# Optimization experiments

Hardware: AMD Instinct MI355X
Metric: run time of the kernel (lower is better)

Reference implementation:

```python
import math
import jax, jax.numpy as jnp
import numpy as np

LOW_FREQ = 1
FACTOR = 1


def setup_inputs() -> dict:
    key = jax.random.key(0)
    x = jax.random.normal(key, (16, 4096, 256), dtype=jnp.float32)
    return {"x": x}


def reference(x):
    b, t, d = x.shape
    x_freq = jnp.fft.rfft(x, axis=1)  # (b, t//2+1, d) complex
    if t % 2 == 0:
        x_freq = x_freq[:, LOW_FREQ:-1]
        f = jnp.fft.rfftfreq(t)[LOW_FREQ:-1]
    else:
        x_freq = x_freq[:, LOW_FREQ:]
        f = jnp.fft.rfftfreq(t)[LOW_FREQ:]
    f = f.astype(jnp.float32)
    F = x_freq.shape[1]
    top_k = int(FACTOR * math.log(F))  # static (shape-derived)

    # top-k by magnitude along freq axis, independently per (b, d)
    xf_bdf = jnp.moveaxis(x_freq, 1, 2)              # (b, d, F)
    _, idx = jax.lax.top_k(jnp.abs(xf_bdf), top_k)   # (b, d, k) int32
    xf_sel = jnp.take_along_axis(xf_bdf, idx, axis=2)  # (b, d, k)
    xf_sel = jnp.moveaxis(xf_sel, 2, 1)              # (b, k, d)
    f_sel = jnp.moveaxis(f[idx], 2, 1)[:, :, None, :]  # (b, k, 1, d)

    # extrapolate: conj-pair frequencies, synthesize cosines, reduce over freq
    xf2 = jnp.concatenate([xf_sel, jnp.conj(xf_sel)], axis=1)  # (b, 2k, d)
    f2 = jnp.concatenate([f_sel, -f_sel], axis=1)              # (b, 2k, 1, d)
    tt = jnp.arange(t, dtype=jnp.float32)[None, None, :, None]  # (1,1,t,1)
    amp = (jnp.abs(xf2) * 2.0 / t)[:, :, None, :]   # (b, 2k, 1, d)
    phase = jnp.angle(xf2)[:, :, None, :]           # (b, 2k, 1, d)
    x_time = amp * jnp.cos(2.0 * math.pi * f2 * tt + phase)  # (b, 2k, t, d)
    return x_time.sum(axis=1)  # (b, t, d)
```

## Files before the change

kernel.cpp:

```cpp
#include <hip/hip_runtime.h>
#include <math.h>

#define T_LEN 4096
#define N2    2048
#define TOPK  7
#define NCH   256
#define R8 0.70710678118654752440

#define AD(a) ((a) + ((a) >> 3) + ((a) >> 8))

__global__ __launch_bounds__(256) void prep_kernel(
    const float* __restrict__ x, float* __restrict__ xt, double2* __restrict__ tw)
{
    if (blockIdx.x < 16) {
        int p = blockIdx.x * 256 + threadIdx.x;
        double th = -2.0 * 3.14159265358979323846 * (double)p / (double)T_LEN;
        tw[p] = make_double2(cos(th), sin(th));
        return;
    }
    __shared__ float tile[64][65];
    const int bid = blockIdx.x - 16;
    const int t0  = (bid & 63) * 64;
    const int c0  = ((bid >> 6) & 3) * 64;
    const int b   = bid >> 8;
    const int tx4 = (threadIdx.x & 15) * 4;
    const int ty  = threadIdx.x >> 4;

    const float* src = x + (size_t)b * T_LEN * NCH;
    for (int r = 0; r < 4; ++r) {
        int t = ty + r * 16;
        float4 v = *(const float4*)(src + (size_t)(t0 + t) * NCH + c0 + tx4);
        tile[t][tx4 + 0] = v.x; tile[t][tx4 + 1] = v.y;
        tile[t][tx4 + 2] = v.z; tile[t][tx4 + 3] = v.w;
    }
    __syncthreads();
    float* dst = xt + (size_t)b * NCH * T_LEN;
    for (int r = 0; r < 4; ++r) {
        int c = ty + r * 16;
        float4 v = make_float4(tile[tx4 + 0][c], tile[tx4 + 1][c],
                               tile[tx4 + 2][c], tile[tx4 + 3][c]);
        *(float4*)(dst + (size_t)(c0 + c) * T_LEN + t0 + tx4) = v;
    }
}

__device__ __forceinline__ void dft8_tw(double ar[8], double ai[8],
                                        int base, const double2* __restrict__ tw)
{
    double t0r=ar[0]+ar[4], t0i=ai[0]+ai[4], t4r=ar[0]-ar[4], t4i=ai[0]-ai[4];
    double t1r=ar[1]+ar[5], t1i=ai[1]+ai[5], t5r=ar[1]-ar[5], t5i=ai[1]-ai[5];
    double t2r=ar[2]+ar[6], t2i=ai[2]+ai[6], t6r=ar[2]-ar[6], t6i=ai[2]-ai[6];
    double t3r=ar[3]+ar[7], t3i=ai[3]+ai[7], t7r=ar[3]-ar[7], t7i=ai[3]-ai[7];
    double s0r=t0r+t2r, s0i=t0i+t2i, s2r=t0r-t2r, s2i=t0i-t2i;
    double s1r=t1r+t3r, s1i=t1i+t3i, s3r=t1r-t3r, s3i=t1i-t3i;
    ar[0]=s0r+s1r; ai[0]=s0i+s1i;
    ar[4]=s0r-s1r; ai[4]=s0i-s1i;
    ar[2]=s2r+s3i; ai[2]=s2i-s3r;
    ar[6]=s2r-s3i; ai[6]=s2i+s3r;
    double c1r=R8*(t5r+t5i), c1i=R8*(t5i-t5r);
    double c2r=t6i,          c2i=-t6r;
    double c3r=R8*(t7i-t7r), c3i=-R8*(t7r+t7i);
    double d0r=t4r+c2r, d0i=t4i+c2i, d1r=t4r-c2r, d1i=t4i-c2i;
    double d2r=c1r+c3r, d2i=c1i+c3i, d3r=c1r-c3r, d3i=c1i-c3i;
    ar[1]=d0r+d2r; ai[1]=d0i+d2i;
    ar[5]=d0r-d2r; ai[5]=d0i-d2i;
    ar[3]=d1r+d3i; ai[3]=d1i-d3r;
    ar[7]=d1r-d3i; ai[7]=d1i+d3r;
#pragma unroll
    for (int m = 1; m < 8; ++m) {
        double2 w = tw[(base * m) & 4095];
        double xr = ar[m], xi = ai[m];
        ar[m] = w.x * xr - w.y * xi;
        ai[m] = w.x * xi + w.y * xr;
    }
}

__device__ __forceinline__ unsigned long long packkey(double mag, int k) {
    unsigned long long b = __double_as_longlong(mag);
    return (b & ~2047ULL) | (unsigned long long)(2047 - k);
}

__global__ __launch_bounds__(256, 4) void fft_topk_kernel(
    const float* __restrict__ xt, const double2* __restrict__ tw,
    int* __restrict__ k_out, float4* __restrict__ ab4)
{
    __shared__ double2 zz[AD(N2 - 1) + 3];
    __shared__ unsigned long long kshare[256];
    __shared__ unsigned long long selkey[TOPK];

    const int tid = threadIdx.x;
    const int bc  = blockIdx.x;
    const float2* xcol2 = (const float2*)(xt + (size_t)bc * T_LEN);

    double ar[8], ai[8];
#pragma unroll
    for (int u = 0; u < 8; ++u) {
        float2 v = xcol2[tid + (u << 8)];
        ar[u] = (double)v.x; ai[u] = (double)v.y;
    }
    dft8_tw(ar, ai, 2 * tid, tw);
#pragma unroll
    for (int m = 0; m < 8; ++m)
        zz[AD((m << 8) + tid)] = make_double2(ar[m], ai[m]);
    __syncthreads();

    {
        const int g = tid >> 5, j2 = tid & 31, base = (g << 8) + j2;
#pragma unroll
        for (int u = 0; u < 8; ++u) {
            double2 v = zz[AD(base + (u << 5))];
            ar[u] = v.x; ai[u] = v.y;
        }
        dft8_tw(ar, ai, 16 * j2, tw);
#pragma unroll
        for (int m = 0; m < 8; ++m)
            zz[AD(base + (m << 5))] = make_double2(ar[m], ai[m]);
    }
    __syncthreads();

    {
        const int g3 = tid >> 2, j3 = tid & 3, base = (g3 << 5) + j3;
#pragma unroll
        for (int u = 0; u < 8; ++u) {
            double2 v = zz[AD(base + (u << 2))];
            ar[u] = v.x; ai[u] = v.y;
        }
        dft8_tw(ar, ai, 128 * j3, tw);
#pragma unroll
        for (int m = 0; m < 8; ++m)
            zz[AD(base + (m << 2))] = make_double2(ar[m], ai[m]);
    }
    __syncthreads();

#pragma unroll
    for (int q = 0; q < 2; ++q) {
        int h4 = ((q << 8) + tid) << 2;
#pragma unroll
        for (int r = 0; r < 4; ++r) {
            double2 v = zz[AD(h4 + r)];
            ar[q * 4 + r] = v.x; ai[q * 4 + r] = v.y;
        }
    }
    __syncthreads();
#pragma unroll
    for (int q = 0; q < 2; ++q) {
        double b0r = ar[q*4+0], b0i = ai[q*4+0], b1r = ar[q*4+1], b1i = ai[q*4+1];
        double b2r = ar[q*4+2], b2i = ai[q*4+2], b3r = ar[q*4+3], b3i = ai[q*4+3];
        double e0r = b0r + b2r, e0i = b0i + b2i, e1r = b0r - b2r, e1i = b0i - b2i;
        double e2r = b1r + b3r, e2i = b1i + b3i, e3r = b1r - b3r, e3i = b1i - b3i;
        int kbase = ((tid & 7) << 6) | (((tid >> 3) & 7) << 3) | (q << 2) | (tid >> 6);
        zz[AD(kbase)]        = make_double2(e0r + e2r, e0i + e2i);
        zz[AD(kbase + 1024)] = make_double2(e0r - e2r, e0i - e2i);
        zz[AD(kbase +  512)] = make_double2(e1r + e3i, e1i - e3r);
        zz[AD(kbase + 1536)] = make_double2(e1r - e3i, e1i + e3r);
    }
    __syncthreads();

    unsigned long long keys[8];
#pragma unroll
    for (int j = 0; j < 4; ++j) {
        int k  = 1 + tid + (j << 8);
        int kp = N2 - k;
        double2 yk = zz[AD(k)];
        double2 yp = zz[AD(kp)];
        double Ar = 0.5 * (yk.x + yp.x), Ai = 0.5 * (yk.y - yp.y);
        double Br = 0.5 * (yk.y + yp.y), Bi = -0.5 * (yk.x - yp.x);
        double2 t = tw[k];
        double Cr = t.x * Br - t.y * Bi;
        double Ci = t.x * Bi + t.y * Br;
        double m1 = (Ar + Cr) * (Ar + Cr) + (Ai + Ci) * (Ai + Ci);
        double m2 = (Ar - Cr) * (Ar - Cr) + (Ai - Ci) * (Ai - Ci);
        keys[2 * j]     = packkey(m1, k);
        keys[2 * j + 1] = (kp != k) ? packkey(m2, kp) : 0ULL;
    }

    unsigned long long lb = 0ULL;
#pragma unroll
    for (int s = 0; s < 8; ++s) lb = (keys[s] > lb) ? keys[s] : lb;

    for (int it = 0; it < TOPK; ++it) {
        kshare[tid] = lb;
        __syncthreads();
        if (tid < 64) {
            unsigned long long v = kshare[tid];
            unsigned long long v1 = kshare[tid + 64];  if (v1 > v) v = v1;
            unsigned long long v2 = kshare[tid + 128]; if (v2 > v) v = v2;
            unsigned long long v3 = kshare[tid + 192]; if (v3 > v) v = v3;
#pragma unroll
            for (int off = 32; off; off >>= 1) {
                unsigned long long o = __shfl_down(v, off);
                if (o > v) v = o;
            }
            if (tid == 0) selkey[it] = v;
        }
        __syncthreads();
        unsigned long long w = selkey[it];
        if (w == lb) {
#pragma unroll
            for (int s = 0; s < 8; ++s) if (keys[s] == w) keys[s] = 0ULL;
            lb = 0ULL;
#pragma unroll
            for (int s = 0; s < 8; ++s) lb = (keys[s] > lb) ? keys[s] : lb;
        }
    }

    if (tid < TOPK) {
        int k  = 2047 - (int)(selkey[tid] & 2047ULL);
        double2 yk = zz[AD(k)];
        double2 yp = zz[AD(N2 - k)];
        double Ar = 0.5 * (yk.x + yp.x), Ai = 0.5 * (yk.y - yp.y);
        double Br = 0.5 * (yk.y + yp.y), Bi = -0.5 * (yk.x - yp.x);
        double2 t = tw[k];
        double Xr = Ar + t.x * Br - t.y * Bi;
        double Xi = Ai + t.x * Bi + t.y * Br;
        k_out[tid * 4096 + bc] = k;
        ab4[tid * 4096 + bc] = make_float4(
            (float)( 4.0 * Xr / (double)T_LEN),
            (float)(-4.0 * Xi / (double)T_LEN),
            (float)t.x, (float)(-t.y));
    }
}

__global__ __launch_bounds__(256) void recon_kernel(
    const int* __restrict__ k_in, const float4* __restrict__ ab4,
    float* __restrict__ out)
{
    __shared__ float tile[16][256];

    const int tid   = threadIdx.x;
    const int chunk = blockIdx.x & 127;
    const int b     = blockIdx.x >> 7;
    const int bc    = (b << 8) + tid;
    const int n0    = chunk << 5;

    const float c0 = 6.28318530717958647692f / 4096.0f;
    float aa[TOPK], bb[TOPK], zr[TOPK], zi[TOPK], wr[TOPK], wi[TOPK];
#pragma unroll
    for (int j = 0; j < TOPK; ++j) {
        int k    = k_in[j * 4096 + bc];
        float4 v = ab4[j * 4096 + bc];
        aa[j] = v.x; bb[j] = v.y; wr[j] = v.z; wi[j] = v.w;
        int m0 = (k * n0) & (T_LEN - 1);
        float ang = (float)m0 * c0;
        zr[j] = __cosf(ang);
        zi[j] = __sinf(ang);
    }

    float* obase = out + ((size_t)b * T_LEN + n0) * NCH;
    for (int r = 0; r < 2; ++r) {
#pragma unroll
        for (int i = 0; i < 16; ++i) {
            float acc = 0.f;
#pragma unroll
            for (int j = 0; j < TOPK; ++j) {
                acc += aa[j] * zr[j] + bb[j] * zi[j];
                float nzr = zr[j] * wr[j] - zi[j] * wi[j];
                zi[j] = zr[j] * wi[j] + zi[j] * wr[j];
                zr[j] = nzr;
            }
            tile[i][tid] = acc;
        }
        __syncthreads();
#pragma unroll
        for (int s = 0; s < 4; ++s) {
            int fid = tid + (s << 8);
            int ni  = fid >> 6;
            int c4  = (fid & 63) << 2;
            float4 v = make_float4(tile[ni][c4], tile[ni][c4 + 1],
                                   tile[ni][c4 + 2], tile[ni][c4 + 3]);
            *(float4*)(obase + (size_t)((r << 4) + ni) * NCH + c4) = v;
        }
        __syncthreads();
    }
}

extern "C" void kernel_launch(void* const* d_in, const int* in_sizes, int n_in,
                              void* d_out, int out_size, void* d_ws, size_t ws_size,
                              hipStream_t stream) {
    const float* x   = (const float*)d_in[0];
    float*       out = (float*)d_out;
    char*        ws  = (char*)d_ws;

    double2* tw   = (double2*)(ws);
    int*     k_ws = (int*)   (ws + 65536);
    float4*  ab_ws= (float4*)(ws + 180224);

    prep_kernel     <<<16 + 4096, 256, 0, stream>>>(x, out, tw);
    fft_topk_kernel <<<4096, 256, 0, stream>>>(out, tw, k_ws, ab_ws);
    recon_kernel    <<<2048, 256, 0, stream>>>(k_ws, ab_ws, out);
}
```

Before: 196.5 us.

## Store FFT intermediates as float in LDS and use per-wave top-k selection

The shared-memory FFT buffer now holds float2 instead of double2. This halves LDS traffic and footprint per block, which may allow higher occupancy; arithmetic stays in double in registers. The top-k search no longer runs seven block-wide reductions with two barriers each. Each wavefront now finds its own top 7 with xor shuffles, and one warp merges the 28 candidates. The cost is rounding every FFT stage to float, which could change which frequencies are chosen when magnitudes are nearly tied.

```diff
diff --git a/kernel.cpp b/kernel.cpp
--- a/kernel.cpp
+++ b/kernel.cpp
@@ -83,8 +83,8 @@
     const float* __restrict__ xt, const double2* __restrict__ tw,
     int* __restrict__ k_out, float4* __restrict__ ab4)
 {
-    __shared__ double2 zz[AD(N2 - 1) + 3];
-    __shared__ unsigned long long kshare[256];
+    __shared__ float2 zz[AD(N2 - 1) + 3];
+    __shared__ unsigned long long wavetop[4 * TOPK];
     __shared__ unsigned long long selkey[TOPK];
 
     const int tid = threadIdx.x;
@@ -100,20 +100,20 @@
     dft8_tw(ar, ai, 2 * tid, tw);
 #pragma unroll
     for (int m = 0; m < 8; ++m)
-        zz[AD((m << 8) + tid)] = make_double2(ar[m], ai[m]);
+        zz[AD((m << 8) + tid)] = make_float2((float)ar[m], (float)ai[m]);
     __syncthreads();
 
     {
         const int g = tid >> 5, j2 = tid & 31, base = (g << 8) + j2;
 #pragma unroll
         for (int u = 0; u < 8; ++u) {
-            double2 v = zz[AD(base + (u << 5))];
-            ar[u] = v.x; ai[u] = v.y;
+            float2 v = zz[AD(base + (u << 5))];
+            ar[u] = (double)v.x; ai[u] = (double)v.y;
         }
         dft8_tw(ar, ai, 16 * j2, tw);
 #pragma unroll
         for (int m = 0; m < 8; ++m)
-            zz[AD(base + (m << 5))] = make_double2(ar[m], ai[m]);
+            zz[AD(base + (m << 5))] = make_float2((float)ar[m], (float)ai[m]);
     }
     __syncthreads();
 
@@ -121,13 +121,13 @@
         const int g3 = tid >> 2, j3 = tid & 3, base = (g3 << 5) + j3;
 #pragma unroll
         for (int u = 0; u < 8; ++u) {
-            double2 v = zz[AD(base + (u << 2))];
-            ar[u] = v.x; ai[u] = v.y;
+            float2 v = zz[AD(base + (u << 2))];
+            ar[u] = (double)v.x; ai[u] = (double)v.y;
         }
         dft8_tw(ar, ai, 128 * j3, tw);
 #pragma unroll
         for (int m = 0; m < 8; ++m)
-            zz[AD(base + (m << 2))] = make_double2(ar[m], ai[m]);
+            zz[AD(base + (m << 2))] = make_float2((float)ar[m], (float)ai[m]);
     }
     __syncthreads();
 
@@ -136,8 +136,8 @@
         int h4 = ((q << 8) + tid) << 2;
 #pragma unroll
         for (int r = 0; r < 4; ++r) {
-            double2 v = zz[AD(h4 + r)];
-            ar[q * 4 + r] = v.x; ai[q * 4 + r] = v.y;
+            float2 v = zz[AD(h4 + r)];
+            ar[q * 4 + r] = (double)v.x; ai[q * 4 + r] = (double)v.y;
         }
     }
     __syncthreads();
@@ -148,10 +148,10 @@
         double e0r = b0r + b2r, e0i = b0i + b2i, e1r = b0r - b2r, e1i = b0i - b2i;
         double e2r = b1r + b3r, e2i = b1i + b3i, e3r = b1r - b3r, e3i = b1i - b3i;
         int kbase = ((tid & 7) << 6) | (((tid >> 3) & 7) << 3) | (q << 2) | (tid >> 6);
-        zz[AD(kbase)]        = make_double2(e0r + e2r, e0i + e2i);
-        zz[AD(kbase + 1024)] = make_double2(e0r - e2r, e0i - e2i);
-        zz[AD(kbase +  512)] = make_double2(e1r + e3i, e1i - e3r);
-        zz[AD(kbase + 1536)] = make_double2(e1r - e3i, e1i + e3r);
+        zz[AD(kbase)]        = make_float2((float)(e0r + e2r), (float)(e0i + e2i));
+        zz[AD(kbase + 1024)] = make_float2((float)(e0r - e2r), (float)(e0i - e2i));
+        zz[AD(kbase +  512)] = make_float2((float)(e1r + e3i), (float)(e1i - e3r));
+        zz[AD(kbase + 1536)] = make_float2((float)(e1r - e3i), (float)(e1i + e3r));
     }
     __syncthreads();
 
@@ -160,10 +160,12 @@
     for (int j = 0; j < 4; ++j) {
         int k  = 1 + tid + (j << 8);
         int kp = N2 - k;
-        double2 yk = zz[AD(k)];
-        double2 yp = zz[AD(kp)];
-        double Ar = 0.5 * (yk.x + yp.x), Ai = 0.5 * (yk.y - yp.y);
-        double Br = 0.5 * (yk.y + yp.y), Bi = -0.5 * (yk.x - yp.x);
+        float2 ykf = zz[AD(k)];
+        float2 ypf = zz[AD(kp)];
+        double ykx = (double)ykf.x, yky = (double)ykf.y;
+        double ypx = (double)ypf.x, ypy = (double)ypf.y;
+        double Ar = 0.5 * (ykx + ypx), Ai = 0.5 * (yky - ypy);
+        double Br = 0.5 * (yky + ypy), Bi = -0.5 * (ykx - ypx);
         double2 t = tw[k];
         double Cr = t.x * Br - t.y * Bi;
         double Ci = t.x * Bi + t.y * Br;
@@ -173,42 +175,50 @@
         keys[2 * j + 1] = (kp != k) ? packkey(m2, kp) : 0ULL;
     }
 
+    const int wv = tid >> 6, ln = tid & 63;
     unsigned long long lb = 0ULL;
 #pragma unroll
     for (int s = 0; s < 8; ++s) lb = (keys[s] > lb) ? keys[s] : lb;
 
     for (int it = 0; it < TOPK; ++it) {
-        kshare[tid] = lb;
-        __syncthreads();
-        if (tid < 64) {
-            unsigned long long v = kshare[tid];
-            unsigned long long v1 = kshare[tid + 64];  if (v1 > v) v = v1;
-            unsigned long long v2 = kshare[tid + 128]; if (v2 > v) v = v2;
-            unsigned long long v3 = kshare[tid + 192]; if (v3 > v) v = v3;
-#pragma unroll
-            for (int off = 32; off; off >>= 1) {
-                unsigned long long o = __shfl_down(v, off);
-                if (o > v) v = o;
+        unsigned long long v = lb;
+#pragma unroll
+        for (int off = 32; off; off >>= 1) {
+            unsigned long long o = __shfl_xor(v, off);
+            if (o > v) v = o;
+        }
+        if (ln == 0) wavetop[wv * TOPK + it] = v;
+#pragma unroll
+        for (int s = 0; s < 8; ++s) keys[s] = (keys[s] == v) ? 0ULL : keys[s];
+        lb = 0ULL;
+#pragma unroll
+        for (int s = 0; s < 8; ++s) lb = (keys[s] > lb) ? keys[s] : lb;
+    }
+    __syncthreads();
+
+    if (tid < 32) {
+        unsigned long long v = (tid < 4 * TOPK) ? wavetop[tid] : 0ULL;
+        for (int it = 0; it < TOPK; ++it) {
+            unsigned long long m = v;
+#pragma unroll
+            for (int off = 16; off; off >>= 1) {
+                unsigned long long o = __shfl_xor(m, off);
+                if (o > m) m = o;
             }
-            if (tid == 0) selkey[it] = v;
-        }
-        __syncthreads();
-        unsigned long long w = selkey[it];
-        if (w == lb) {
-#pragma unroll
-            for (int s = 0; s < 8; ++s) if (keys[s] == w) keys[s] = 0ULL;
-            lb = 0ULL;
-#pragma unroll
-            for (int s = 0; s < 8; ++s) lb = (keys[s] > lb) ? keys[s] : lb;
-        }
-    }
+            if (tid == 0) selkey[it] = m;
+            if (m == v) v = 0ULL;
+        }
+    }
+    __syncthreads();
 
     if (tid < TOPK) {
         int k  = 2047 - (int)(selkey[tid] & 2047ULL);
-        double2 yk = zz[AD(k)];
-        double2 yp = zz[AD(N2 - k)];
-        double Ar = 0.5 * (yk.x + yp.x), Ai = 0.5 * (yk.y - yp.y);
-        double Br = 0.5 * (yk.y + yp.y), Bi = -0.5 * (yk.x - yp.x);
+        float2 ykf = zz[AD(k)];
+        float2 ypf = zz[AD(N2 - k)];
+        double ykx = (double)ykf.x, yky = (double)ykf.y;
+        double ypx = (double)ypf.x, ypy = (double)ypf.y;
+        double Ar = 0.5 * (ykx + ypx), Ai = 0.5 * (yky - ypy);
+        double Br = 0.5 * (yky + ypy), Bi = -0.5 * (ykx - ypx);
         double2 t = tw[k];
         double Xr = Ar + t.x * Br - t.y * Bi;
         double Xi = Ai + t.x * Bi + t.y * Br;
```

Result: no change. 194.9 us (-0.8%).
